# Optimization experiments

Measured on AMD Instinct MI355X. Metric: run time of the kernel, lower is better.

The kernel has to match this reference:

```python
import jax, jax.numpy as jnp
import numpy as np

V, E, H, P, L, NH = 10000, 512, 512, 512, 2, 8
B, T, S = 32, 128, 512
SOS = 1
HD = H // NH  # head dim


def setup_inputs() -> dict:
    key = jax.random.key(0)
    ks = jax.random.split(key, 12)
    s = 0.02
    emb = jax.random.normal(ks[0], (V, E)) * s
    emb = emb.at[0].set(0.0)  # padding_idx=0
    Wih = jax.random.normal(ks[1], (L, 4 * H, E)) * s
    Whh = jax.random.normal(ks[2], (L, 4 * H, H)) * s
    bih = jnp.zeros((L, 4 * H), jnp.float32)
    bhh = jnp.zeros((L, 4 * H), jnp.float32)
    in_proj_w = jax.random.normal(ks[3], (3 * H, H)) * s
    in_proj_b = jnp.zeros((3 * H,), jnp.float32)
    out_w = jax.random.normal(ks[4], (H, H)) * s
    out_b = jnp.zeros((H,), jnp.float32)
    proj_w = jax.random.normal(ks[5], (P, H)) * s
    gen_w = jax.random.normal(ks[6], (V, P)) * s
    inputs = jax.random.randint(ks[7], (B, T), 3, V, dtype=jnp.int32)  # avoid pad/sos/eos
    encoder_outputs = jax.random.normal(ks[8], (B, S, H))
    return {"inputs": inputs, "encoder_outputs": encoder_outputs, "emb": emb,
            "Wih": Wih, "Whh": Whh, "bih": bih, "bhh": bhh,
            "in_proj_w": in_proj_w, "in_proj_b": in_proj_b,
            "out_w": out_w, "out_b": out_b, "proj_w": proj_w, "gen_w": gen_w,
            "teacher_forcing_ratio": 1, "return_decode_dict": 0}


def _lstm(seq, Wih, Whh, bih, bhh):
    # seq: [T1, B, E]; multi-layer LSTM, PyTorch gate order i,f,g,o
    Bx = seq.shape[1]
    for l in range(Wih.shape[0]):
        def step(carry, xt, Wi=Wih[l], Wh=Whh[l], b=bih[l] + bhh[l]):
            h, c = carry
            g = xt @ Wi.T + h @ Wh.T + b
            i, f, gg, o = jnp.split(g, 4, axis=-1)
            c = jax.nn.sigmoid(f) * c + jax.nn.sigmoid(i) * jnp.tanh(gg)
            h = jax.nn.sigmoid(o) * jnp.tanh(c)
            return (h, c), h
        init = (jnp.zeros((Bx, H), seq.dtype), jnp.zeros((Bx, H), seq.dtype))
        _, seq = jax.lax.scan(step, init, seq)
    return seq  # [T1, B, H]


def reference(inputs, encoder_outputs, emb, Wih, Whh, bih, bhh,
              in_proj_w, in_proj_b, out_w, out_b, proj_w, gen_w,
              teacher_forcing_ratio, return_decode_dict):
    Bx, Tx = inputs.shape
    # prepend <sos>  (teacher-forcing branch, ratio=1.0 -> always taken)
    toks = jnp.concatenate([jnp.full((Bx, 1), SOS, inputs.dtype), inputs], axis=1)  # [B,T+1]
    x = emb[toks]                      # embedding (dropout_p=0 -> identity)
    seq = _lstm(x.transpose(1, 0, 2), Wih, Whh, bih, bhh)   # [T1,B,H]
    # MultiheadAttention: query=decoder out, key/value=encoder outputs
    kv = encoder_outputs.transpose(1, 0, 2)                 # [S,B,H]
    Wq, Wk, Wv = jnp.split(in_proj_w, 3, axis=0)
    bq, bk, bv = jnp.split(in_proj_b, 3, axis=0)
    q = (seq @ Wq.T + bq).reshape(-1, Bx, NH, HD) * (HD ** -0.5)  # [T1,B,NH,HD]
    k = (kv @ Wk.T + bk).reshape(S, Bx, NH, HD)
    v = (kv @ Wv.T + bv).reshape(S, Bx, NH, HD)
    scores = jnp.einsum('tbhd,sbhd->bhts', q, k)            # [B,NH,T1,S]
    attn = jax.nn.softmax(scores, axis=-1)
    ctx = jnp.einsum('bhts,sbhd->tbhd', attn, v).reshape(-1, Bx, H)
    ctx = ctx @ out_w.T + out_b                             # [T1,B,H]
    out = ctx.transpose(1, 0, 2)                            # [B,T1,H]
    logits = (out @ proj_w.T) @ gen_w.T                     # [B,T1,V]
    return jax.nn.log_softmax(logits, axis=-1)
```

## Files before the change

### kernel.cpp

```cpp
#include <hip/hip_runtime.h>
#include <cstdint>

typedef unsigned short u16;
typedef unsigned int u32;
typedef __attribute__((ext_vector_type(8))) short bf16x8;
typedef __attribute__((ext_vector_type(4))) float f32x4;

#define DI __device__ __forceinline__

constexpr int VV = 10000, E = 512, H = 512, NH = 8, HD = 64;
constexpr int B = 32, T = 128, S = 512, T1 = 129;
constexpr int G4 = 2048;
constexpr int M_ROWS = T1 * B;
constexpr int NWG_LSTM = 64;

DI u16 f2bf(float f) {
  uint32_t u = __builtin_bit_cast(uint32_t, f);
  u = (u + 0x7FFF + ((u >> 16) & 1)) >> 16;
  return (u16)u;
}
DI float sigm(float x) { return 1.f / (1.f + __expf(-x)); }
DI float tanh_(float x) { return 1.f - 2.f / (__expf(2.f * x) + 1.f); }

DI f32x4 MFMA(bf16x8 a, bf16x8 b, f32x4 c) {
  return __builtin_amdgcn_mfma_f32_16x16x32_bf16(a, b, c, 0, 0, 0);
}

#define GLD_LDS(gptr, lptr)                                                     \
  __builtin_amdgcn_global_load_lds(                                             \
      (const __attribute__((address_space(1))) uint32_t*)(const void*)(gptr),   \
      (__attribute__((address_space(3))) uint32_t*)(void*)(lptr), 16, 0, 0)

__global__ __launch_bounds__(256) void k_convert(const float* __restrict__ src,
                                                 u16* __restrict__ dst, int n4) {
  int i = blockIdx.x * 256 + threadIdx.x;
  int stride = gridDim.x * 256;
  for (; i < n4; i += stride) {
    float4 v = ((const float4*)src)[i];
    ushort4 o;
    o.x = f2bf(v.x); o.y = f2bf(v.y); o.z = f2bf(v.z); o.w = f2bf(v.w);
    ((ushort4*)dst)[i] = o;
  }
}

__global__ __launch_bounds__(256) void k_embed(const int* __restrict__ toks,
                                               const float* __restrict__ emb,
                                               u16* __restrict__ out) {
  int idx = blockIdx.x * 256 + threadIdx.x;
  int total = T1 * B * (E / 4);
  if (idx >= total) return;
  int ch = idx & (E / 4 - 1);
  int r = idx / (E / 4);
  int t = r >> 5, b = r & 31;
  int tok = (t == 0) ? 1 : toks[b * T + (t - 1)];
  float4 v = ((const float4*)(emb + (size_t)tok * E))[ch];
  ushort4 o;
  o.x = f2bf(v.x); o.y = f2bf(v.y); o.z = f2bf(v.z); o.w = f2bf(v.w);
  ((ushort4*)out)[idx] = o;
}

template <int MODE>
__global__ __launch_bounds__(256) void k_gemm(const u16* __restrict__ A,
                                              const u16* __restrict__ Bm,
                                              const float* __restrict__ bias,
                                              const float* __restrict__ bias2,
                                              void* __restrict__ Cout, int M, int N,
                                              float scale) {
  __shared__ __align__(16) u16 As[128 * 64];
  __shared__ __align__(16) u16 Bs[128 * 64];
  const int tid = threadIdx.x, lane = tid & 63, wid = tid >> 6;
  const int wm = wid >> 1, wn = wid & 1;
  const int r0 = blockIdx.y * 128, n0 = blockIdx.x * 128;
  f32x4 acc[4][4] = {};
  const int brow = wid * 32;

  for (int k0 = 0; k0 < 512; k0 += 64) {
    for (int q = 0; q < 4; q++) {
      int row_l = brow + q * 8 + (lane >> 3);
      int slot = lane & 7;
      int scol = (slot ^ (row_l & 7)) * 8;
      int ra = r0 + row_l; if (ra > M - 1) ra = M - 1;
      GLD_LDS(A + (size_t)ra * 512 + k0 + scol, &As[(brow + q * 8) * 64]);
      int rb = n0 + row_l; if (rb > N - 1) rb = N - 1;
      GLD_LDS(Bm + (size_t)rb * 512 + k0 + scol, &Bs[(brow + q * 8) * 64]);
    }
    __syncthreads();
    for (int ks = 0; ks < 2; ks++) {
      bf16x8 af[4], bf[4];
      for (int mt = 0; mt < 4; mt++) {
        int row = wm * 64 + mt * 16 + (lane & 15);
        int slot = (ks * 4 + (lane >> 4)) ^ (row & 7);
        af[mt] = *(const bf16x8*)&As[row * 64 + slot * 8];
      }
      for (int nt = 0; nt < 4; nt++) {
        int row = wn * 64 + nt * 16 + (lane & 15);
        int slot = (ks * 4 + (lane >> 4)) ^ (row & 7);
        bf[nt] = *(const bf16x8*)&Bs[row * 64 + slot * 8];
      }
      for (int mt = 0; mt < 4; mt++)
        for (int nt = 0; nt < 4; nt++)
          acc[mt][nt] = MFMA(af[mt], bf[nt], acc[mt][nt]);
    }
    __syncthreads();
  }

  for (int mt = 0; mt < 4; mt++)
    for (int nt = 0; nt < 4; nt++) {
      int c = n0 + wn * 64 + nt * 16 + (lane & 15);
      float bv = 0.f;
      if (c < N) {
        if (bias) bv += bias[c];
        if (bias2) bv += bias2[c];
      }
      for (int rg = 0; rg < 4; rg++) {
        int r = r0 + wm * 64 + mt * 16 + (lane >> 4) * 4 + rg;
        if (r >= M || c >= N) continue;
        float v = acc[mt][nt][rg];
        if constexpr (MODE == 0) {
          int t = r >> 5, b = r & 31;
          ((float*)Cout)[((size_t)t * G4 + c) * 32 + b] = v + bv;
        } else if constexpr (MODE == 1) {
          ((u16*)Cout)[(size_t)r * N + c] = f2bf(v + bv);
        } else if constexpr (MODE == 2) {
          int t = r >> 5, b = r & 31, h = c >> 6, d = c & 63;
          ((u16*)Cout)[((size_t)(b * NH + h) * T1 + t) * HD + d] = f2bf((v + bv) * scale);
        } else if constexpr (MODE == 3) {
          int b = r >> 9, s = r & 511, h = c >> 6, d = c & 63;
          ((u16*)Cout)[((size_t)(b * NH + h) * HD + d) * S + s] = f2bf(v + bv);
        } else {
          int t = r >> 5, b = r & 31;
          ((float*)Cout)[((size_t)b * T1 + t) * VV + c] = v;
        }
      }
    }
}

__global__ __launch_bounds__(256) void k_lstm2(const float* __restrict__ G0,
                                               const u16* __restrict__ Whh0,
                                               const u16* __restrict__ Wih1,
                                               const u16* __restrict__ Whh1,
                                               const float* __restrict__ bih1,
                                               const float* __restrict__ bhh1,
                                               u16* __restrict__ seq1,
                                               u16* __restrict__ hbuf,
                                               u32* __restrict__ flags) {
  __shared__ __align__(16) u16 hA[32 * 512];
  __shared__ __align__(16) u16 hX[32 * 512];
  float* xchg = (float*)hA;
  u16* hx = (u16*)hA + 4352;
  const int tid = threadIdx.x, lane = tid & 63, g = tid >> 6;
  const int wg = blockIdx.x;
  const bool isL1 = wg >= 32;
  const int u0 = (isL1 ? wg - 32 : wg) * 16;

  u16* hb0 = hbuf;
  u16* hb1 = hbuf + 2 * 32 * 512;

  bf16x8 afh[16], afx[16];
  {
    const u16* Wh = isL1 ? Whh1 : Whh0;
    int row = g * 512 + u0 + (lane & 15);
    const u16* wp = Wh + (size_t)row * 512 + (lane >> 4) * 8;
    for (int ks = 0; ks < 16; ks++) afh[ks] = *(const bf16x8*)(wp + ks * 32);
    if (isL1) {
      const u16* xp = Wih1 + (size_t)row * 512 + (lane >> 4) * 8;
      for (int ks = 0; ks < 16; ks++) afx[ks] = *(const bf16x8*)(xp + ks * 32);
    }
  }
  float bsum[2][4];
  if (isL1) {
    for (int j = 0; j < 2; j++) {
      int uu = (tid + 256 * j) >> 5;
      for (int gg = 0; gg < 4; gg++)
        bsum[j][gg] = bih1[gg * 512 + u0 + uu] + bhh1[gg * 512 + u0 + uu];
    }
  }
  float cst[2] = {0.f, 0.f};

  for (int u = 0; u < 130; u++) {
    const int t = isL1 ? (u - 1) : u;
    const bool active = isL1 ? (u >= 1) : (u < 129);

    if (active) {
      float gpre[2][4];
      if (!isL1) {
        for (int j = 0; j < 2; j++) {
          int p = tid + 256 * j; int b = p & 31, uu = p >> 5;
          const float* Gp = G0 + ((size_t)t * G4 + u0 + uu) * 32 + b;
          gpre[j][0] = Gp[0];         gpre[j][1] = Gp[512 * 32];
          gpre[j][2] = Gp[1024 * 32]; gpre[j][3] = Gp[1536 * 32];
        }
      }
      {
        uint4 z = {0, 0, 0, 0};
        const u16* srcA = isL1 ? (hb1 + (size_t)(t & 1) * (32 * 512))
                               : (hb0 + (size_t)(t & 1) * (32 * 512));
        const u16* srcX = hb0 + (size_t)(u & 1) * (32 * 512);
        for (int j = 0; j < 8; j++) {
          int cid = tid + 256 * j;
          int row = cid >> 6, slot = cid & 63;
          int dsto = row * 512 + ((slot ^ (row & 7)) * 8);
          if (t == 0) *(uint4*)&hA[dsto] = z;
          else        *(uint4*)&hA[dsto] = *(const uint4*)&srcA[row * 512 + slot * 8];
          if (isL1)   *(uint4*)&hX[dsto] = *(const uint4*)&srcX[row * 512 + slot * 8];
        }
      }
      __syncthreads();
      f32x4 acc[2] = {};
      for (int ks = 0; ks < 16; ks++)
        for (int nt = 0; nt < 2; nt++) {
          int row = nt * 16 + (lane & 15);
          int off = row * 512 + (((ks * 4 + (lane >> 4)) ^ (row & 7)) * 8);
          acc[nt] = MFMA(afh[ks], *(const bf16x8*)&hA[off], acc[nt]);
          if (isL1) acc[nt] = MFMA(afx[ks], *(const bf16x8*)&hX[off], acc[nt]);
        }
      __syncthreads();
      for (int nt = 0; nt < 2; nt++)
        for (int rg = 0; rg < 4; rg++)
          xchg[(g * 32 + nt * 16 + (lane & 15)) * 17 + (lane >> 4) * 4 + rg] = acc[nt][rg];
      __syncthreads();
      for (int j = 0; j < 2; j++) {
        int p = tid + 256 * j; int b = p & 31, uu = p >> 5;
        float gi, gf, gg_, go;
        if (!isL1) { gi = gpre[j][0]; gf = gpre[j][1]; gg_ = gpre[j][2]; go = gpre[j][3]; }
        else       { gi = bsum[j][0]; gf = bsum[j][1]; gg_ = bsum[j][2]; go = bsum[j][3]; }
        float i_ = sigm(xchg[(0 * 32 + b) * 17 + uu] + gi);
        float f_ = sigm(xchg[(1 * 32 + b) * 17 + uu] + gf);
        float g_ = tanh_(xchg[(2 * 32 + b) * 17 + uu] + gg_);
        float o_ = sigm(xchg[(3 * 32 + b) * 17 + uu] + go);
        float c = f_ * cst[j] + i_ * g_;
        cst[j] = c;
        hx[b * 16 + uu] = f2bf(o_ * tanh_(c));
      }
      __syncthreads();
      if (tid < 32) {
        uint4 v0 = *(const uint4*)&hx[tid * 16];
        uint4 v1 = *(const uint4*)&hx[tid * 16 + 8];
        u16* hd = (isL1 ? hb1 : hb0) + (size_t)((t + 1) & 1) * (32 * 512) + (size_t)tid * 512 + u0;
        *(uint4*)hd = v0; *(uint4*)(hd + 8) = v1;
        if (isL1) {
          u16* sd = seq1 + ((size_t)t * 32 + tid) * 512 + u0;
          *(uint4*)sd = v0; *(uint4*)(sd + 8) = v1;
        }
      }
    }
    __syncthreads();
    if (tid == 0) {
      __threadfence();
      __hip_atomic_store(&flags[wg], (u32)(u + 1), __ATOMIC_RELEASE, __HIP_MEMORY_SCOPE_AGENT);
    }
    if (tid < NWG_LSTM) {
      while (__hip_atomic_load(&flags[tid], __ATOMIC_ACQUIRE, __HIP_MEMORY_SCOPE_AGENT) <= (u32)u)
        __builtin_amdgcn_s_sleep(1);
    }
    __syncthreads();
  }
}

__global__ __launch_bounds__(256) void k_attn(const u16* __restrict__ Q,
                                              const u16* __restrict__ Kall,
                                              const u16* __restrict__ Vt,
                                              u16* __restrict__ ctx) {
  __shared__ __align__(16) u16 p_lds[32 * 520];
  __shared__ float red[4][32], red2[4][32], rsum[32];
  const int bid = blockIdx.x;
  const int tt = bid % 5, h = (bid / 5) & 7, b = bid / 40;
  const int tid = threadIdx.x, lane = tid & 63, w = tid >> 6;

  bf16x8 qf[2][2];
  for (int mt = 0; mt < 2; mt++)
    for (int ks = 0; ks < 2; ks++) {
      int t = tt * 32 + mt * 16 + (lane & 15);
      if (t > 128) t = 128;
      qf[mt][ks] = *(const bf16x8*)&Q[((size_t)(b * NH + h) * T1 + t) * HD + ks * 32 + (lane >> 4) * 8];
    }

  f32x4 sc[8][2] = {};
  for (int j = 0; j < 8; j++) {
    int nt = w + 4 * j;
    for (int ks = 0; ks < 2; ks++) {
      int srow = nt * 16 + (lane & 15);
      bf16x8 kf = *(const bf16x8*)&Kall[(size_t)(b * S + srow) * H + h * HD + ks * 32 + (lane >> 4) * 8];
      for (int mt = 0; mt < 2; mt++) sc[j][mt] = MFMA(qf[mt][ks], kf, sc[j][mt]);
    }
  }
  for (int mt = 0; mt < 2; mt++)
    for (int rg = 0; rg < 4; rg++) {
      float m = -1e30f;
      for (int j = 0; j < 8; j++) m = fmaxf(m, sc[j][mt][rg]);
      for (int mk = 1; mk < 16; mk <<= 1) m = fmaxf(m, __shfl_xor(m, mk));
      if ((lane & 15) == 0) red[w][mt * 16 + (lane >> 4) * 4 + rg] = m;
    }
  __syncthreads();
  for (int mt = 0; mt < 2; mt++)
    for (int rg = 0; rg < 4; rg++) {
      int row = mt * 16 + (lane >> 4) * 4 + rg;
      float M = fmaxf(fmaxf(red[0][row], red[1][row]), fmaxf(red[2][row], red[3][row]));
      float s = 0.f;
      for (int j = 0; j < 8; j++) {
        float p = __expf(sc[j][mt][rg] - M);
        s += p;
        p_lds[row * 520 + (w + 4 * j) * 16 + (lane & 15)] = f2bf(p);
      }
      for (int mk = 1; mk < 16; mk <<= 1) s += __shfl_xor(s, mk);
      if ((lane & 15) == 0) red2[w][row] = s;
    }
  __syncthreads();
  if (tid < 32) rsum[tid] = red2[0][tid] + red2[1][tid] + red2[2][tid] + red2[3][tid];

  f32x4 pacc[2] = {};
  {
    int nt = w;
    for (int ks = 0; ks < 16; ks++) {
      bf16x8 vf = *(const bf16x8*)&Vt[((size_t)(b * NH + h) * HD + nt * 16 + (lane & 15)) * S + ks * 32 + (lane >> 4) * 8];
      for (int mt = 0; mt < 2; mt++) {
        bf16x8 pf = *(const bf16x8*)&p_lds[(mt * 16 + (lane & 15)) * 520 + ks * 32 + (lane >> 4) * 8];
        pacc[mt] = MFMA(pf, vf, pacc[mt]);
      }
    }
  }
  __syncthreads();
  for (int mt = 0; mt < 2; mt++)
    for (int rg = 0; rg < 4; rg++) {
      int lrow = mt * 16 + (lane >> 4) * 4 + rg;
      int trow = tt * 32 + lrow;
      if (trow < T1) {
        float v = pacc[mt][rg] / rsum[lrow];
        ctx[((size_t)trow * 32 + b) * H + h * HD + w * 16 + (lane & 15)] = f2bf(v);
      }
    }
}

__global__ __launch_bounds__(256) void k_lsm(float* __restrict__ out) {
  float* p = out + (size_t)blockIdx.x * VV;
  const int tid = threadIdx.x;
  float m = -1e30f, s = 0.f;
  for (int i = tid; i < VV; i += 256) {
    float v = p[i];
    if (v > m) { s *= __expf(m - v); m = v; }
    s += __expf(v - m);
  }
  for (int off = 32; off; off >>= 1) {
    float m2 = __shfl_xor(m, off), s2 = __shfl_xor(s, off);
    float M = fmaxf(m, m2);
    s = s * __expf(m - M) + s2 * __expf(m2 - M);
    m = M;
  }
  __shared__ float wm[4], ws[4];
  if ((tid & 63) == 0) { wm[tid >> 6] = m; ws[tid >> 6] = s; }
  __syncthreads();
  float M = fmaxf(fmaxf(wm[0], wm[1]), fmaxf(wm[2], wm[3]));
  float Sv = ws[0] * __expf(wm[0] - M) + ws[1] * __expf(wm[1] - M) +
             ws[2] * __expf(wm[2] - M) + ws[3] * __expf(wm[3] - M);
  float lse = M + __logf(Sv);
  for (int i = tid; i < VV; i += 256) p[i] -= lse;
}

extern "C" void kernel_launch(void* const* d_in, const int* in_sizes, int n_in,
                              void* d_out, int out_size, void* d_ws, size_t ws_size,
                              hipStream_t stream) {
  const int* inputs = (const int*)d_in[0];
  const float* enc = (const float*)d_in[1];
  const float* emb = (const float*)d_in[2];
  const float* Wih = (const float*)d_in[3];
  const float* Whh = (const float*)d_in[4];
  const float* bih = (const float*)d_in[5];
  const float* bhh = (const float*)d_in[6];
  const float* ipw = (const float*)d_in[7];
  const float* ipb = (const float*)d_in[8];
  const float* outw = (const float*)d_in[9];
  const float* outb = (const float*)d_in[10];
  const float* projw = (const float*)d_in[11];
  const float* genw = (const float*)d_in[12];
  float* out = (float*)d_out;

  char* wp = (char*)d_ws;
  auto alloc = [&](size_t bytes) {
    char* p = wp;
    wp += (bytes + 255) & ~(size_t)255;
    return p;
  };
  u16* embx = (u16*)alloc((size_t)M_ROWS * E * 2);
  u16* seq1 = (u16*)alloc((size_t)M_ROWS * H * 2);
  u16* WihB = (u16*)alloc((size_t)2 * G4 * E * 2);
  u16* WhhB = (u16*)alloc((size_t)2 * G4 * H * 2);
  u16* ipwB = (u16*)alloc((size_t)3 * H * H * 2);
  u16* outwB = (u16*)alloc((size_t)H * H * 2);
  u16* projwB = (u16*)alloc((size_t)H * H * 2);
  u16* genwB = (u16*)alloc((size_t)VV * H * 2);
  u16* encB = (u16*)alloc((size_t)B * S * H * 2);
  u16* hbuf = (u16*)alloc((size_t)4 * 32 * 512 * 2);
  u32* flags = (u32*)alloc(256);
  float* Gbuf = (float*)alloc((size_t)T1 * G4 * 32 * 4);
  u16* Qb = (u16*)alloc((size_t)B * NH * T1 * HD * 2);
  u16* ctxb = (u16*)alloc((size_t)M_ROWS * H * 2);
  u16* Kall = (u16*)Gbuf;
  u16* Vtb = (u16*)((char*)Gbuf + (size_t)B * S * H * 2);
  u16* attout = encB;
  u16* hidden = (u16*)((char*)encB + (size_t)M_ROWS * H * 2);

  k_convert<<<1024, 256, 0, stream>>>(Wih, WihB, 2 * G4 * E / 4);
  k_convert<<<1024, 256, 0, stream>>>(Whh, WhhB, 2 * G4 * H / 4);
  k_convert<<<1024, 256, 0, stream>>>(ipw, ipwB, 3 * H * H / 4);
  k_convert<<<1024, 256, 0, stream>>>(outw, outwB, H * H / 4);
  k_convert<<<1024, 256, 0, stream>>>(projw, projwB, H * H / 4);
  k_convert<<<1024, 256, 0, stream>>>(genw, genwB, VV * H / 4);
  k_convert<<<1024, 256, 0, stream>>>(enc, encB, B * S * H / 4);
  k_embed<<<(M_ROWS * (E / 4) + 255) / 256, 256, 0, stream>>>(inputs, emb, embx);
  hipMemsetAsync(flags, 0, 256, stream);

  k_gemm<0><<<dim3(16, 33), 256, 0, stream>>>(embx, WihB, bih, bhh, Gbuf, M_ROWS, G4, 1.f);

  {
    const float* g0 = Gbuf;
    const u16* wh0 = WhhB;
    const u16* wi1 = WihB + (size_t)G4 * E;
    const u16* wh1 = WhhB + (size_t)G4 * H;
    const float* b1i = bih + G4;
    const float* b1h = bhh + G4;
    u16* sq = seq1; u16* hb = hbuf; u32* fl = flags;
    void* args[] = {&g0, &wh0, &wi1, &wh1, &b1i, &b1h, &sq, &hb, &fl};
    hipLaunchCooperativeKernel((void*)k_lstm2, dim3(NWG_LSTM), dim3(256), args, 0, stream);
  }

  k_gemm<1><<<dim3(4, 128), 256, 0, stream>>>(encB, ipwB + (size_t)H * H, ipb + H, nullptr,
                                              Kall, B * S, H, 1.f);
  k_gemm<3><<<dim3(4, 128), 256, 0, stream>>>(encB, ipwB + (size_t)2 * H * H, ipb + 2 * H, nullptr,
                                              Vtb, B * S, H, 1.f);
  k_gemm<2><<<dim3(4, 33), 256, 0, stream>>>(seq1, ipwB, ipb, nullptr, Qb, M_ROWS, H, 0.125f);

  k_attn<<<B * NH * 5, 256, 0, stream>>>(Qb, Kall, Vtb, ctxb);

  k_gemm<1><<<dim3(4, 33), 256, 0, stream>>>(ctxb, outwB, outb, nullptr, attout, M_ROWS, H, 1.f);
  k_gemm<1><<<dim3(4, 33), 256, 0, stream>>>(attout, projwB, nullptr, nullptr, hidden, M_ROWS, H, 1.f);
  k_gemm<4><<<dim3(79, 33), 256, 0, stream>>>(hidden, genwB, nullptr, nullptr, out, M_ROWS, VV, 1.f);

  k_lsm<<<M_ROWS, 256, 0, stream>>>(out);

  (void)in_sizes; (void)n_in; (void)out_size; (void)ws_size;
}
```

Baseline: 2.070 ms.

## Relax LSTM inter-workgroup sync with relaxed atomics and merge conversion kernels

Replaces the per-step release/acquire flag handshake and threadfence in the persistent LSTM kernel with relaxed agent-scope atomic loads and stores of the hidden state, plus an explicit vmcnt wait before raising the flag. It also drops the barrier before the flag store and lengthens the spin sleep. Separately, the seven fp32-to-bf16 conversion launches become a single kernel driven by a job table. The aim is to shorten the serial per-timestep synchronisation latency and cut launch overhead, but relaxed ordering makes the memory-ordering correctness of the hidden-state exchange rely on hardware behaviour.

New measurement: 1.980 ms. -4.3%, faster.

```diff
diff --git a/kernel.cpp b/kernel.cpp
--- a/kernel.cpp
+++ b/kernel.cpp
@@ -26,20 +26,34 @@
   return __builtin_amdgcn_mfma_f32_16x16x32_bf16(a, b, c, 0, 0, 0);
 }
 
+DI u32 aload(const u32* p) {
+  return __hip_atomic_load((u32*)p, __ATOMIC_RELAXED, __HIP_MEMORY_SCOPE_AGENT);
+}
+DI void astore(u32* p, u32 v) {
+  __hip_atomic_store(p, v, __ATOMIC_RELAXED, __HIP_MEMORY_SCOPE_AGENT);
+}
+
 #define GLD_LDS(gptr, lptr)                                                     \
   __builtin_amdgcn_global_load_lds(                                             \
       (const __attribute__((address_space(1))) uint32_t*)(const void*)(gptr),   \
       (__attribute__((address_space(3))) uint32_t*)(void*)(lptr), 16, 0, 0)
 
-__global__ __launch_bounds__(256) void k_convert(const float* __restrict__ src,
-                                                 u16* __restrict__ dst, int n4) {
+struct CJobs {
+  const float* s[7];
+  u16* d[7];
+  int n4[7];
+  int tot;
+};
+__global__ __launch_bounds__(256) void k_convert_all(CJobs j) {
   int i = blockIdx.x * 256 + threadIdx.x;
   int stride = gridDim.x * 256;
-  for (; i < n4; i += stride) {
-    float4 v = ((const float4*)src)[i];
+  for (; i < j.tot; i += stride) {
+    int rem = i, k = 0;
+    while (rem >= j.n4[k]) { rem -= j.n4[k]; k++; }
+    float4 v = ((const float4*)j.s[k])[rem];
     ushort4 o;
     o.x = f2bf(v.x); o.y = f2bf(v.y); o.z = f2bf(v.z); o.w = f2bf(v.w);
-    ((ushort4*)dst)[i] = o;
+    ((ushort4*)j.d[k])[rem] = o;
   }
 }
 
@@ -191,18 +205,35 @@
           gpre[j][2] = Gp[1024 * 32]; gpre[j][3] = Gp[1536 * 32];
         }
       }
-      {
-        uint4 z = {0, 0, 0, 0};
-        const u16* srcA = isL1 ? (hb1 + (size_t)(t & 1) * (32 * 512))
-                               : (hb0 + (size_t)(t & 1) * (32 * 512));
-        const u16* srcX = hb0 + (size_t)(u & 1) * (32 * 512);
+      u32 va[8][4], vx[8][4];
+      const u16* srcA = isL1 ? (hb1 + (size_t)(t & 1) * (32 * 512))
+                             : (hb0 + (size_t)(t & 1) * (32 * 512));
+      const u16* srcX = hb0 + (size_t)(u & 1) * (32 * 512);
+      if (t > 0) {
         for (int j = 0; j < 8; j++) {
           int cid = tid + 256 * j;
-          int row = cid >> 6, slot = cid & 63;
-          int dsto = row * 512 + ((slot ^ (row & 7)) * 8);
-          if (t == 0) *(uint4*)&hA[dsto] = z;
-          else        *(uint4*)&hA[dsto] = *(const uint4*)&srcA[row * 512 + slot * 8];
-          if (isL1)   *(uint4*)&hX[dsto] = *(const uint4*)&srcX[row * 512 + slot * 8];
+          const u32* ps = (const u32*)(srcA + (cid >> 6) * 512 + (cid & 63) * 8);
+          for (int q = 0; q < 4; q++) va[j][q] = aload(ps + q);
+        }
+      }
+      if (isL1) {
+        for (int j = 0; j < 8; j++) {
+          int cid = tid + 256 * j;
+          const u32* ps = (const u32*)(srcX + (cid >> 6) * 512 + (cid & 63) * 8);
+          for (int q = 0; q < 4; q++) vx[j][q] = aload(ps + q);
+        }
+      }
+      for (int j = 0; j < 8; j++) {
+        int cid = tid + 256 * j;
+        int row = cid >> 6, slot = cid & 63;
+        int dsto = row * 512 + ((slot ^ (row & 7)) * 8);
+        uint4 w;
+        if (t == 0) { w.x = 0; w.y = 0; w.z = 0; w.w = 0; }
+        else { w.x = va[j][0]; w.y = va[j][1]; w.z = va[j][2]; w.w = va[j][3]; }
+        *(uint4*)&hA[dsto] = w;
+        if (isL1) {
+          uint4 x; x.x = vx[j][0]; x.y = vx[j][1]; x.z = vx[j][2]; x.w = vx[j][3];
+          *(uint4*)&hX[dsto] = x;
         }
       }
       __syncthreads();
@@ -234,24 +265,22 @@
       }
       __syncthreads();
       if (tid < 32) {
-        uint4 v0 = *(const uint4*)&hx[tid * 16];
-        uint4 v1 = *(const uint4*)&hx[tid * 16 + 8];
-        u16* hd = (isL1 ? hb1 : hb0) + (size_t)((t + 1) & 1) * (32 * 512) + (size_t)tid * 512 + u0;
-        *(uint4*)hd = v0; *(uint4*)(hd + 8) = v1;
+        const u32* hs = (const u32*)&hx[tid * 16];
+        u16* hd = (isL1 ? hb1 : hb0) + (size_t)((t + 1) & 1) * (32 * 512) +
+                  (size_t)tid * 512 + u0;
+        u32* hd32 = (u32*)hd;
+        for (int q = 0; q < 8; q++) astore(hd32 + q, hs[q]);
         if (isL1) {
           u16* sd = seq1 + ((size_t)t * 32 + tid) * 512 + u0;
-          *(uint4*)sd = v0; *(uint4*)(sd + 8) = v1;
-        }
-      }
-    }
-    __syncthreads();
-    if (tid == 0) {
-      __threadfence();
-      __hip_atomic_store(&flags[wg], (u32)(u + 1), __ATOMIC_RELEASE, __HIP_MEMORY_SCOPE_AGENT);
-    }
+          *(uint4*)sd = *(const uint4*)&hx[tid * 16];
+          *(uint4*)(sd + 8) = *(const uint4*)&hx[tid * 16 + 8];
+        }
+      }
+    }
+    asm volatile("s_waitcnt vmcnt(0)" ::: "memory");
+    if (tid == 0) astore(&flags[wg], (u32)(u + 1));
     if (tid < NWG_LSTM) {
-      while (__hip_atomic_load(&flags[tid], __ATOMIC_ACQUIRE, __HIP_MEMORY_SCOPE_AGENT) <= (u32)u)
-        __builtin_amdgcn_s_sleep(1);
+      while (aload(&flags[tid]) <= (u32)u) __builtin_amdgcn_s_sleep(2);
     }
     __syncthreads();
   }
@@ -399,13 +428,19 @@
   u16* attout = encB;
   u16* hidden = (u16*)((char*)encB + (size_t)M_ROWS * H * 2);
 
-  k_convert<<<1024, 256, 0, stream>>>(Wih, WihB, 2 * G4 * E / 4);
-  k_convert<<<1024, 256, 0, stream>>>(Whh, WhhB, 2 * G4 * H / 4);
-  k_convert<<<1024, 256, 0, stream>>>(ipw, ipwB, 3 * H * H / 4);
-  k_convert<<<1024, 256, 0, stream>>>(outw, outwB, H * H / 4);
-  k_convert<<<1024, 256, 0, stream>>>(projw, projwB, H * H / 4);
-  k_convert<<<1024, 256, 0, stream>>>(genw, genwB, VV * H / 4);
-  k_convert<<<1024, 256, 0, stream>>>(enc, encB, B * S * H / 4);
+  {
+    CJobs cj;
+    cj.s[0] = Wih;  cj.d[0] = WihB;  cj.n4[0] = 2 * G4 * E / 4;
+    cj.s[1] = Whh;  cj.d[1] = WhhB;  cj.n4[1] = 2 * G4 * H / 4;
+    cj.s[2] = ipw;  cj.d[2] = ipwB;  cj.n4[2] = 3 * H * H / 4;
+    cj.s[3] = outw; cj.d[3] = outwB; cj.n4[3] = H * H / 4;
+    cj.s[4] = projw; cj.d[4] = projwB; cj.n4[4] = H * H / 4;
+    cj.s[5] = genw; cj.d[5] = genwB; cj.n4[5] = VV * H / 4;
+    cj.s[6] = enc;  cj.d[6] = encB;  cj.n4[6] = B * S * H / 4;
+    cj.tot = 0;
+    for (int k = 0; k < 7; k++) cj.tot += cj.n4[k];
+    k_convert_all<<<1024, 256, 0, stream>>>(cj);
+  }
   k_embed<<<(M_ROWS * (E / 4) + 255) / 256, 256, 0, stream>>>(inputs, emb, embx);
   hipMemsetAsync(flags, 0, 256, stream);
 
```
